# Kernel optimization log

Measured on AMD Instinct MI355X. Metric: run time of the kernel, lower is better.

The kernel has to match this reference:

```python
import jax, jax.numpy as jnp
import numpy as np

N = 100_000   # nodes
E = 640_000   # edges
H = 128       # hidden_dim
L = 4         # num_layers
C = 2         # num_classes
G = 128       # graphs in batch

def setup_inputs() -> dict:
    key = jax.random.key(0)
    ks = jax.random.split(key, 8)
    x = jax.random.randint(ks[0], (N, 1), 0, 2)
    edge_index = jax.random.randint(ks[1], (2, E), 0, N)
    batch = jnp.sort(jax.random.randint(ks[2], (N,), 0, G))
    embed = jax.random.normal(ks[3], (2, H), jnp.float32)
    Ws = jax.random.normal(ks[4], (L, H, H), jnp.float32) * (1.0 / np.sqrt(H))
    bs = jnp.zeros((L, H), jnp.float32)
    W_out = jax.random.normal(ks[5], (H, C), jnp.float32) * (1.0 / np.sqrt(H))
    b_out = jnp.zeros((C,), jnp.float32)
    return dict(x=x, edge_index=edge_index, batch=batch, embed=embed,
                Ws=Ws, bs=bs, W_out=W_out, b_out=b_out)

def reference(x, edge_index, batch, embed, Ws, bs, W_out, b_out):
    src, dst = edge_index[0], edge_index[1]
    # symmetric GCN normalization with self-loops (PyG GCNConv default)
    deg = jax.ops.segment_sum(jnp.ones(E, jnp.float32), dst, num_segments=N) + 1.0
    dinv = jax.lax.rsqrt(deg)
    enorm = (dinv[src] * dinv[dst])[:, None]   # per-edge norm
    snorm = (dinv * dinv)[:, None]             # self-loop norm

    h = embed[x[:, 0]]                          # [N, H] embedding lookup
    n_layers = Ws.shape[0]
    for l in range(n_layers):
        t = h @ Ws[l]                           # linear transform [N, H]
        agg = jax.ops.segment_sum(t[src] * enorm, dst, num_segments=N) \
              + t * snorm + bs[l]
        h = jax.nn.relu(agg) if l < n_layers - 1 else agg

    # global mean pool over graph ids
    counts = jax.ops.segment_sum(jnp.ones(N, jnp.float32), batch, num_segments=G)
    pooled = jax.ops.segment_sum(h, batch, num_segments=G) \
             / jnp.maximum(counts, 1.0)[:, None]   # [G, H]
    return pooled @ W_out + b_out                  # [G, C]
```

## Files before the change

kernel.cpp:

```cpp
#include <hip/hip_runtime.h>

typedef __attribute__((ext_vector_type(8))) short bf16x8;
typedef __attribute__((ext_vector_type(4))) float f32x4;
typedef __attribute__((ext_vector_type(2))) float f32x2;

__device__ inline unsigned short bf16_rtn(float f) {
  unsigned u = __float_as_uint(f);
  unsigned r = u + 0x7fffu + ((u >> 16) & 1u);
  return (unsigned short)(r >> 16);
}

__device__ inline void split_bf16(float f, unsigned short& hi, unsigned short& lo) {
  hi = bf16_rtn(f);
  float fh = __uint_as_float((unsigned)hi << 16);
  lo = bf16_rtn(f - fh);
}

__device__ inline float bf16_to_f(unsigned short v) {
  return __uint_as_float((unsigned)v << 16);
}

__device__ inline unsigned char f_to_fp8(float f) {
  int r = __builtin_amdgcn_cvt_pk_fp8_f32(f, f, 0, false);
  return (unsigned char)(r & 0xff);
}
__device__ inline f32x2 fp8x2_to_f(unsigned short v) {
  return __builtin_amdgcn_cvt_pk_f32_fp8((int)v, false);
}

__global__ void k_init(int* __restrict__ deg, int* __restrict__ gpz, int N, int M,
                       const float* __restrict__ Ws, const float* __restrict__ embed,
                       unsigned short* __restrict__ wphi,
                       unsigned short* __restrict__ wplo,
                       float* __restrict__ T,
                       unsigned char* __restrict__ t_a,
                       unsigned char* __restrict__ t_b) {
  int i = blockIdx.x * 256 + threadIdx.x;
  if (i < N) deg[i] = 0;
  if (i < M) gpz[i] = 0;
  int l = blockIdx.x;
  if (l < 3) {
    const float* W = Ws + (size_t)(l + 1) * 128 * 128;
    unsigned short* dh = wphi + (size_t)l * 16384;
    unsigned short* dl = wplo + (size_t)l * 16384;
    for (int idx = threadIdx.x; idx < 16384; idx += 256) {
      int j = idx & 7;
      int lane = (idx >> 3) & 63;
      int c = (idx >> 9) & 3;
      int ct = idx >> 11;
      int k = c * 32 + ((lane >> 4) * 8) + j;
      int n = ct * 16 + (lane & 15);
      unsigned short hi, lo;
      split_bf16(W[k * 128 + n], hi, lo);
      dh[idx] = hi;
      dl[idx] = lo;
    }
  } else if (l == 3) {
    int t = threadIdx.x;
    int r = t >> 7, c = t & 127;
    float acc = 0.f;
    for (int k = 0; k < 128; ++k)
      acc += embed[r * 128 + k] * Ws[k * 128 + c];
    T[r * 128 + c] = acc;
  } else if (l == 4) {
    int t = threadIdx.x;
    if (t < 32)      ((unsigned*)(t_a + (size_t)N * 128))[t] = 0u;
    else if (t < 64) ((unsigned*)(t_b + (size_t)N * 128))[t - 32] = 0u;
  }
}


__global__ void k_hist(const int* __restrict__ dst, int* __restrict__ deg,
                       int* __restrict__ posr, int E) {
  int e = blockIdx.x * 256 + threadIdx.x;
  if (e < E) posr[e] = atomicAdd(&deg[dst[e]], 1);
}

__global__ void k_scan1(const int* __restrict__ deg, int* __restrict__ rowptr,
                        int* __restrict__ bsum, float* __restrict__ dpk,
                        const int* __restrict__ x, const int* __restrict__ batch,
                        int* __restrict__ gstart, int* __restrict__ gend, int N) {
  __shared__ int s[256];
  int t = threadIdx.x;
  int i = blockIdx.x * 256 + t;
  int v = (i < N) ? deg[i] : 0;
  if (i < N) {
    float di = rsqrtf((float)v + 1.0f);
    dpk[i] = x[i] ? -di : di;
    int g = batch[i];
    if (i == 0 || batch[i - 1] != g) gstart[g] = i;
    if (i == N - 1 || batch[i + 1] != g) gend[g] = i + 1;
  }
  s[t] = v;
  __syncthreads();
  for (int off = 1; off < 256; off <<= 1) {
    int u = (t >= off) ? s[t - off] : 0;
    __syncthreads();
    s[t] += u;
    __syncthreads();
  }
  if (i < N) rowptr[i] = s[t] - v;
  if (t == 255) bsum[blockIdx.x] = s[255];
}

__global__ void k_scan2(const int* __restrict__ bsum, int* __restrict__ boff, int nb) {
  __shared__ int s[512];
  int t = threadIdx.x;
  int v = (t < nb) ? bsum[t] : 0;
  s[t] = v;
  __syncthreads();
  for (int off = 1; off < 512; off <<= 1) {
    int u = (t >= off) ? s[t - off] : 0;
    __syncthreads();
    s[t] += u;
    __syncthreads();
  }
  boff[t] = s[t] - v;
}

__global__ void k_scan3(int* __restrict__ rowptr, const int* __restrict__ boff,
                        int N, int E) {
  int i = blockIdx.x * 256 + threadIdx.x;
  if (i < N) rowptr[i] += boff[i >> 8];
  if (i == 0) rowptr[N] = E;
}

__global__ void k_scatter(const int* __restrict__ src, const int* __restrict__ dst,
                          const int* __restrict__ posr, const int* __restrict__ rowptr,
                          const float* __restrict__ dpk,
                          int2* __restrict__ epack, int E) {
  int e = blockIdx.x * 256 + threadIdx.x;
  if (e >= E) return;
  int s = src[e], d = dst[e];
  int pos = rowptr[d] + posr[e];
  epack[pos] = make_int2(s, __float_as_int(dpk[s]));
}


__device__ inline void acc16(float* a, uint4 p) {
  f32x2 v;
  v = __builtin_amdgcn_cvt_pk_f32_fp8((int)p.x, false); a[0]  += v.x; a[1]  += v.y;
  v = __builtin_amdgcn_cvt_pk_f32_fp8((int)p.x, true);  a[2]  += v.x; a[3]  += v.y;
  v = __builtin_amdgcn_cvt_pk_f32_fp8((int)p.y, false); a[4]  += v.x; a[5]  += v.y;
  v = __builtin_amdgcn_cvt_pk_f32_fp8((int)p.y, true);  a[6]  += v.x; a[7]  += v.y;
  v = __builtin_amdgcn_cvt_pk_f32_fp8((int)p.z, false); a[8]  += v.x; a[9]  += v.y;
  v = __builtin_amdgcn_cvt_pk_f32_fp8((int)p.z, true);  a[10] += v.x; a[11] += v.y;
  v = __builtin_amdgcn_cvt_pk_f32_fp8((int)p.w, false); a[12] += v.x; a[13] += v.y;
  v = __builtin_amdgcn_cvt_pk_f32_fp8((int)p.w, true);  a[14] += v.x; a[15] += v.y;
}

__device__ inline void gather8(const unsigned char* __restrict__ tin,
                               const int2* __restrict__ epack,
                               int r0, int deg, int l8, int N,
                               float* a) {
  int dcap = deg < 16 ? deg : 16;
  int slo = N, shi = N;
  if (2 * l8 < dcap)     slo = epack[r0 + 2 * l8].x;
  if (2 * l8 + 1 < dcap) shi = epack[r0 + 2 * l8 + 1].x;

  uint4 p[16];
  #pragma unroll
  for (int k = 0; k < 8; ++k) {
    int se = __shfl(slo, k, 8);
    int so = __shfl(shi, k, 8);
    p[2 * k]     = *(const uint4*)(tin + (size_t)((unsigned)se * 128u + ((unsigned)l8 << 4)));
    p[2 * k + 1] = *(const uint4*)(tin + (size_t)((unsigned)so * 128u + ((unsigned)l8 << 4)));
  }
  #pragma unroll
  for (int k = 0; k < 16; ++k) acc16(a, p[k]);

  if (__builtin_expect(deg > 16, 0)) {
    for (int e = r0 + 16; e < r0 + deg; ++e) {
      int s = epack[e].x;
      uint4 q = *(const uint4*)(tin + (size_t)((unsigned)s * 128u + ((unsigned)l8 << 4)));
      acc16(a, q);
    }
  }
}

__global__ __launch_bounds__(256)
void k_agg(const unsigned char* __restrict__ tin,
           const int* __restrict__ rowptr,
           const int2* __restrict__ epack,
           const float* __restrict__ dpk, const float* __restrict__ bvec,
           unsigned short* __restrict__ h, int N) {
  int lane = threadIdx.x & 63;
  int g8 = lane >> 3, l8 = lane & 7;
  int wid = (blockIdx.x * 256 + threadIdx.x) >> 6;
  int i = wid * 8 + g8;
  if (i >= N) return;
  int r0 = rowptr[i], r1 = rowptr[i + 1];
  uint4 ps = *(const uint4*)(tin + (size_t)i * 128 + (l8 << 4));
  float dp = dpk[i];

  float a[16];
  #pragma unroll
  for (int k = 0; k < 16; ++k) a[k] = 0.f;
  gather8(tin, epack, r0, r1 - r0, l8, N, a);
  acc16(a, ps);

  float di = fabsf(dp);
  const float4* bp = (const float4*)(bvec + 16 * l8);
  float4 b0 = bp[0], b1 = bp[1], b2 = bp[2], b3 = bp[3];
  float bb[16] = {b0.x, b0.y, b0.z, b0.w, b1.x, b1.y, b1.z, b1.w,
                  b2.x, b2.y, b2.z, b2.w, b3.x, b3.y, b3.z, b3.w};
  unsigned u[8];
  #pragma unroll
  for (int k = 0; k < 8; ++k) {
    float v0 = fmaxf(di * a[2 * k]     + bb[2 * k],     0.f);
    float v1 = fmaxf(di * a[2 * k + 1] + bb[2 * k + 1], 0.f);
    u[k] = (unsigned)bf16_rtn(v0) | ((unsigned)bf16_rtn(v1) << 16);
  }
  uint4* hp = (uint4*)(h + (size_t)i * 128 + 16 * l8);
  hp[0] = make_uint4(u[0], u[1], u[2], u[3]);
  hp[1] = make_uint4(u[4], u[5], u[6], u[7]);
}

__global__ __launch_bounds__(256)
void k_agg_pool(const unsigned char* __restrict__ tin,
                const int* __restrict__ rowptr,
                const int2* __restrict__ epack,
                const float* __restrict__ dpk, const float* __restrict__ bvec,
                const int* __restrict__ batch,
                float* __restrict__ pooled, int N) {
  __shared__ float sh[32][128];
  __shared__ int sg[32];
  int lane = threadIdx.x & 63;
  int g8 = lane >> 3, l8 = lane & 7;
  int nloc = (threadIdx.x >> 6) * 8 + g8;
  int i = blockIdx.x * 32 + nloc;
  if (threadIdx.x < 32) sg[threadIdx.x] = -1;
  __syncthreads();
  if (i < N) {
    int r0 = rowptr[i], r1 = rowptr[i + 1];
    uint4 ps = *(const uint4*)(tin + (size_t)i * 128 + (l8 << 4));
    float dp = dpk[i];

    float a[16];
    #pragma unroll
    for (int k = 0; k < 16; ++k) a[k] = 0.f;
    gather8(tin, epack, r0, r1 - r0, l8, N, a);
    acc16(a, ps);

    float di = fabsf(dp);
    const float4* bp = (const float4*)(bvec + 16 * l8);
    float4 b0 = bp[0], b1 = bp[1], b2 = bp[2], b3 = bp[3];
    float bb[16] = {b0.x, b0.y, b0.z, b0.w, b1.x, b1.y, b1.z, b1.w,
                    b2.x, b2.y, b2.z, b2.w, b3.x, b3.y, b3.z, b3.w};
    #pragma unroll
    for (int k = 0; k < 16; ++k)
      sh[nloc][16 * l8 + k] = di * a[k] + bb[k];
    if (l8 == 0) sg[nloc] = batch[i];
  }
  __syncthreads();
  if (threadIdx.x < 128) {
    int c = threadIdx.x;
    float acc = 0.f;
    int cur = sg[0];
    #pragma unroll
    for (int w2 = 0; w2 < 32; ++w2) {
      int gw = sg[w2];
      if (gw < 0) break;
      if (gw != cur) {
        atomicAdd(&pooled[cur * 128 + c], acc);
        acc = 0.f;
        cur = gw;
      }
      acc += sh[w2][c];
    }
    atomicAdd(&pooled[cur * 128 + c], acc);
  }
}

__global__ void k_gemm(const unsigned short* __restrict__ h,
                       const unsigned short* __restrict__ wphi,
                       const unsigned short* __restrict__ wplo,
                       const float* __restrict__ dpk,
                       unsigned char* __restrict__ tout, int N) {
  int wave = threadIdx.x >> 6;
  int lane = threadIdx.x & 63;
  int r0 = (blockIdx.x * 4 + wave) * 32;
  if (r0 >= N) return;
  int q = lane >> 4;
  int m = lane & 15;
  const bf16x8* bh_base = (const bf16x8*)wphi;
  const bf16x8* bl_base = (const bf16x8*)wplo;

  f32x4 acc[2][8];
  #pragma unroll
  for (int tt = 0; tt < 2; ++tt)
    #pragma unroll
    for (int ct = 0; ct < 8; ++ct)
      acc[tt][ct] = (f32x4){0.f, 0.f, 0.f, 0.f};

  for (int c = 0; c < 4; ++c) {
    bf16x8 a0 = *(const bf16x8*)(h + (size_t)(r0 + m) * 128 + c * 32 + q * 8);
    bf16x8 a1 = *(const bf16x8*)(h + (size_t)(r0 + 16 + m) * 128 + c * 32 + q * 8);
    #pragma unroll
    for (int ct = 0; ct < 8; ++ct) {
      bf16x8 bh = bh_base[(ct * 4 + c) * 64 + lane];
      bf16x8 bl = bl_base[(ct * 4 + c) * 64 + lane];
      acc[0][ct] = __builtin_amdgcn_mfma_f32_16x16x32_bf16(a0, bh, acc[0][ct], 0, 0, 0);
      acc[0][ct] = __builtin_amdgcn_mfma_f32_16x16x32_bf16(a0, bl, acc[0][ct], 0, 0, 0);
      acc[1][ct] = __builtin_amdgcn_mfma_f32_16x16x32_bf16(a1, bh, acc[1][ct], 0, 0, 0);
      acc[1][ct] = __builtin_amdgcn_mfma_f32_16x16x32_bf16(a1, bl, acc[1][ct], 0, 0, 0);
    }
  }

  #pragma unroll
  for (int tt = 0; tt < 2; ++tt)
    #pragma unroll
    for (int ct = 0; ct < 8; ++ct)
      #pragma unroll
      for (int r = 0; r < 4; ++r) {
        int row = r0 + tt * 16 + q * 4 + r;
        if (row < N) {
          float sc = fabsf(dpk[row]);
          tout[(size_t)row * 128 + ct * 16 + m] = f_to_fp8(sc * acc[tt][ct][r]);
        }
      }
}

__device__ inline void gemm_tile8(const unsigned short* hT,
                                  const unsigned short* __restrict__ wphi,
                                  const unsigned short* __restrict__ wplo,
                                  const float* __restrict__ dpk,
                                  unsigned char* __restrict__ tout, int i0, int N) {
  int ct = threadIdx.x >> 6;
  int lane = threadIdx.x & 63;
  int q = lane >> 4;
  int m = lane & 15;
  const bf16x8* bh_base = (const bf16x8*)wphi;
  const bf16x8* bl_base = (const bf16x8*)wplo;

  f32x4 acc0 = (f32x4){0.f, 0.f, 0.f, 0.f};
  f32x4 acc1 = (f32x4){0.f, 0.f, 0.f, 0.f};

  #pragma unroll
  for (int c = 0; c < 4; ++c) {
    bf16x8 a0 = *(const bf16x8*)(hT + (m) * 136 + c * 32 + q * 8);
    bf16x8 a1 = *(const bf16x8*)(hT + (16 + m) * 136 + c * 32 + q * 8);
    bf16x8 bh = bh_base[(ct * 4 + c) * 64 + lane];
    bf16x8 bl = bl_base[(ct * 4 + c) * 64 + lane];
    acc0 = __builtin_amdgcn_mfma_f32_16x16x32_bf16(a0, bh, acc0, 0, 0, 0);
    acc0 = __builtin_amdgcn_mfma_f32_16x16x32_bf16(a0, bl, acc0, 0, 0, 0);
    acc1 = __builtin_amdgcn_mfma_f32_16x16x32_bf16(a1, bh, acc1, 0, 0, 0);
    acc1 = __builtin_amdgcn_mfma_f32_16x16x32_bf16(a1, bl, acc1, 0, 0, 0);
  }

  #pragma unroll
  for (int r = 0; r < 4; ++r) {
    int row0 = i0 + q * 4 + r;
    int row1 = row0 + 16;
    if (row0 < N) {
      float sc = fabsf(dpk[row0]);
      tout[(size_t)row0 * 128 + ct * 16 + m] = f_to_fp8(sc * acc0[r]);
    }
    if (row1 < N) {
      float sc = fabsf(dpk[row1]);
      tout[(size_t)row1 * 128 + ct * 16 + m] = f_to_fp8(sc * acc1[r]);
    }
  }
}

__global__ __launch_bounds__(512)
void k_l1_gemm(const int* __restrict__ rowptr,
               const int2* __restrict__ epack,
               const float* __restrict__ dpk, const float* __restrict__ T,
               const float* __restrict__ b0,
               const unsigned short* __restrict__ wphi,
               const unsigned short* __restrict__ wplo,
               unsigned char* __restrict__ tout, int N) {
  __shared__ unsigned short hT[32 * 136];
  int wave = threadIdx.x >> 6;
  int lane = threadIdx.x & 63;
  int i0 = blockIdx.x * 32;

  for (int j = wave * 4; j < wave * 4 + 4; ++j) {
    int i = i0 + j;
    if (i >= N) break;
    int r0 = rowptr[i], r1 = rowptr[i + 1];
    float sabs = 0.f, sneg = 0.f;
    for (int e = r0 + lane; e < r1; e += 64) {
      float wv = __int_as_float(epack[e].y);
      float aw = fabsf(wv);
      sabs += aw;
      if (wv < 0.f) sneg += aw;
    }
    for (int mm = 32; mm >= 1; mm >>= 1) {
      sabs += __shfl_xor(sabs, mm, 64);
      sneg += __shfl_xor(sneg, mm, 64);
    }
    float dp = dpk[i];
    float di = fabsf(dp);
    float sn = di * di;
    float c1 = di * sneg;
    float c0 = di * (sabs - sneg);
    if (dp < 0.f) c1 += sn; else c0 += sn;
    float v0 = fmaxf(c0 * T[2 * lane]     + c1 * T[128 + 2 * lane]     + b0[2 * lane],     0.f);
    float v1 = fmaxf(c0 * T[2 * lane + 1] + c1 * T[128 + 2 * lane + 1] + b0[2 * lane + 1], 0.f);
    *(unsigned*)&hT[j * 136 + 2 * lane] = (unsigned)bf16_rtn(v0) | ((unsigned)bf16_rtn(v1) << 16);
  }
  __syncthreads();
  gemm_tile8(hT, wphi, wplo, dpk, tout, i0, N);
}

__global__ void k_out(const float* __restrict__ pooled, const int* __restrict__ gstart,
                      const int* __restrict__ gend, const float* __restrict__ W_out,
                      const float* __restrict__ b_out, float* __restrict__ out, int G) {
  __shared__ float sp[128];
  int g = blockIdx.x;
  int j = threadIdx.x;
  float cnt = (float)(gend[g] - gstart[g]);
  sp[j] = pooled[g * 128 + j] / fmaxf(cnt, 1.f);
  __syncthreads();
  if (j < 2) {
    float o = b_out[j];
    for (int k = 0; k < 128; ++k)
      o += sp[k] * W_out[k * 2 + j];
    out[g * 2 + j] = o;
  }
}

extern "C" void kernel_launch(void* const* d_in, const int* in_sizes, int n_in,
                              void* d_out, int out_size, void* d_ws, size_t ws_size,
                              hipStream_t stream) {
  const int*   x     = (const int*)d_in[0];
  const int*   ei    = (const int*)d_in[1];
  const int*   batch = (const int*)d_in[2];
  const float* embed = (const float*)d_in[3];
  const float* Ws    = (const float*)d_in[4];
  const float* bs    = (const float*)d_in[5];
  const float* W_out = (const float*)d_in[6];
  const float* b_out = (const float*)d_in[7];
  float* out = (float*)d_out;

  int N = in_sizes[2];
  int E = in_sizes[1] / 2;
  int G = out_size / 2;

  const int* src = ei;
  const int* dst = ei + E;

  char* w = (char*)d_ws;
  auto alloc = [&](size_t bytes) {
    char* p = w;
    w += (bytes + 255) & ~(size_t)255;
    return p;
  };
  int*   deg    = (int*)  alloc((size_t)N * 4);
  float* dpk    = (float*)alloc((size_t)N * 4);
  int*   rowptr = (int*)  alloc((size_t)(N + 1) * 4);
  int*   posr   = (int*)  alloc((size_t)E * 4);
  int*   bsum   = (int*)  alloc(512 * 4);
  int*   boff   = (int*)  alloc(512 * 4);
  int*   gstart = (int*)  alloc((size_t)G * 4);
  int*   gend   = (int*)  alloc((size_t)G * 4);
  float* pooled = (float*)alloc((size_t)G * 128 * 4);
  float* T      = (float*)alloc(256 * 4);
  unsigned short* wphi = (unsigned short*)alloc((size_t)3 * 16384 * 2);
  unsigned short* wplo = (unsigned short*)alloc((size_t)3 * 16384 * 2);
  int2*  epack  = (int2*) alloc((size_t)E * 8);
  unsigned short* h = (unsigned short*)alloc((size_t)N * 128 * 2);
  unsigned char* t_a = (unsigned char*)alloc((size_t)(N + 1) * 128);
  unsigned char* t_b = (unsigned char*)alloc((size_t)(N + 1) * 128);

  int nbN = (N + 255) / 256;
  int nbE = (E + 255) / 256;
  int ntile = (N + 31) / 32;
  int nagg = (N + 31) / 32;
  int ngemm = (N + 127) / 128;
  int M = G * 130;

  k_init<<<nbN, 256, 0, stream>>>(deg, gstart, N, M, Ws, embed, wphi, wplo, T, t_a, t_b);
  k_hist<<<nbE, 256, 0, stream>>>(dst, deg, posr, E);
  k_scan1<<<nbN, 256, 0, stream>>>(deg, rowptr, bsum, dpk, x, batch, gstart, gend, N);
  k_scan2<<<1, 512, 0, stream>>>(bsum, boff, nbN);
  k_scan3<<<nbN, 256, 0, stream>>>(rowptr, boff, N, E);
  k_scatter<<<nbE, 256, 0, stream>>>(src, dst, posr, rowptr, dpk, epack, E);

  k_l1_gemm<<<ntile, 512, 0, stream>>>(rowptr, epack, dpk, T, bs,
                                       wphi, wplo, t_a, N);
  k_agg<<<nagg, 256, 0, stream>>>(t_a, rowptr, epack, dpk, bs + 128, h, N);
  k_gemm<<<ngemm, 256, 0, stream>>>(h, wphi + 16384, wplo + 16384, dpk, t_b, N);
  k_agg<<<nagg, 256, 0, stream>>>(t_b, rowptr, epack, dpk, bs + 256, h, N);
  k_gemm<<<ngemm, 256, 0, stream>>>(h, wphi + 32768, wplo + 32768, dpk, t_a, N);
  k_agg_pool<<<nagg, 256, 0, stream>>>(t_a, rowptr, epack, dpk, bs + 384,
                                       batch, pooled, N);
  k_out<<<G, 128, 0, stream>>>(pooled, gstart, gend, W_out, b_out, out, G);
}
```

Measured before the change: 288.1 us.

## Fuse aggregation and next-layer GEMM via shared-memory tile of h

Merges the per-layer aggregation kernel with the following linear-transform GEMM. Each block aggregates 32 nodes, writes the bf16 activations to a padded LDS tile, then four waves each compute two 16-column output tiles with MFMA and write fp8 results. This removes the global round trip of the bf16 h buffer and two kernel launches per forward pass. In exchange, every block re-reads the weight fragments and there is a block-wide barrier between gather and GEMM.

```diff
diff --git a/kernel.cpp b/kernel.cpp
--- a/kernel.cpp
+++ b/kernel.cpp
@@ -179,41 +179,97 @@
 }
 
 __global__ __launch_bounds__(256)
-void k_agg(const unsigned char* __restrict__ tin,
-           const int* __restrict__ rowptr,
-           const int2* __restrict__ epack,
-           const float* __restrict__ dpk, const float* __restrict__ bvec,
-           unsigned short* __restrict__ h, int N) {
+void k_agg_gemm(const unsigned char* __restrict__ tin,
+                const int* __restrict__ rowptr,
+                const int2* __restrict__ epack,
+                const float* __restrict__ dpk, const float* __restrict__ bvec,
+                const unsigned short* __restrict__ wphi,
+                const unsigned short* __restrict__ wplo,
+                unsigned char* __restrict__ tout, int N) {
+  __shared__ unsigned short hT[32 * 136];
   int lane = threadIdx.x & 63;
+  int wave = threadIdx.x >> 6;
   int g8 = lane >> 3, l8 = lane & 7;
-  int wid = (blockIdx.x * 256 + threadIdx.x) >> 6;
-  int i = wid * 8 + g8;
-  if (i >= N) return;
-  int r0 = rowptr[i], r1 = rowptr[i + 1];
-  uint4 ps = *(const uint4*)(tin + (size_t)i * 128 + (l8 << 4));
-  float dp = dpk[i];
-
-  float a[16];
-  #pragma unroll
-  for (int k = 0; k < 16; ++k) a[k] = 0.f;
-  gather8(tin, epack, r0, r1 - r0, l8, N, a);
-  acc16(a, ps);
-
-  float di = fabsf(dp);
-  const float4* bp = (const float4*)(bvec + 16 * l8);
-  float4 b0 = bp[0], b1 = bp[1], b2 = bp[2], b3 = bp[3];
-  float bb[16] = {b0.x, b0.y, b0.z, b0.w, b1.x, b1.y, b1.z, b1.w,
-                  b2.x, b2.y, b2.z, b2.w, b3.x, b3.y, b3.z, b3.w};
+  int nloc = wave * 8 + g8;
+  int i0 = blockIdx.x * 32;
+  int i = i0 + nloc;
+
   unsigned u[8];
-  #pragma unroll
-  for (int k = 0; k < 8; ++k) {
-    float v0 = fmaxf(di * a[2 * k]     + bb[2 * k],     0.f);
-    float v1 = fmaxf(di * a[2 * k + 1] + bb[2 * k + 1], 0.f);
-    u[k] = (unsigned)bf16_rtn(v0) | ((unsigned)bf16_rtn(v1) << 16);
-  }
-  uint4* hp = (uint4*)(h + (size_t)i * 128 + 16 * l8);
-  hp[0] = make_uint4(u[0], u[1], u[2], u[3]);
-  hp[1] = make_uint4(u[4], u[5], u[6], u[7]);
+  if (i < N) {
+    int r0 = rowptr[i], r1 = rowptr[i + 1];
+    uint4 ps = *(const uint4*)(tin + (size_t)i * 128 + (l8 << 4));
+    float dp = dpk[i];
+
+    float a[16];
+    #pragma unroll
+    for (int k = 0; k < 16; ++k) a[k] = 0.f;
+    gather8(tin, epack, r0, r1 - r0, l8, N, a);
+    acc16(a, ps);
+
+    float di = fabsf(dp);
+    const float4* bp = (const float4*)(bvec + 16 * l8);
+    float4 b0 = bp[0], b1 = bp[1], b2 = bp[2], b3 = bp[3];
+    float bb[16] = {b0.x, b0.y, b0.z, b0.w, b1.x, b1.y, b1.z, b1.w,
+                    b2.x, b2.y, b2.z, b2.w, b3.x, b3.y, b3.z, b3.w};
+    #pragma unroll
+    for (int k = 0; k < 8; ++k) {
+      float v0 = fmaxf(di * a[2 * k]     + bb[2 * k],     0.f);
+      float v1 = fmaxf(di * a[2 * k + 1] + bb[2 * k + 1], 0.f);
+      u[k] = (unsigned)bf16_rtn(v0) | ((unsigned)bf16_rtn(v1) << 16);
+    }
+  } else {
+    #pragma unroll
+    for (int k = 0; k < 8; ++k) u[k] = 0u;
+  }
+  {
+    uint4* hp = (uint4*)&hT[nloc * 136 + 16 * l8];
+    hp[0] = make_uint4(u[0], u[1], u[2], u[3]);
+    hp[1] = make_uint4(u[4], u[5], u[6], u[7]);
+  }
+  __syncthreads();
+
+  int q = lane >> 4;
+  int m = lane & 15;
+  const bf16x8* bh_base = (const bf16x8*)wphi;
+  const bf16x8* bl_base = (const bf16x8*)wplo;
+
+  f32x4 acc[2][2];
+  #pragma unroll
+  for (int tt = 0; tt < 2; ++tt)
+    #pragma unroll
+    for (int ctl = 0; ctl < 2; ++ctl)
+      acc[tt][ctl] = (f32x4){0.f, 0.f, 0.f, 0.f};
+
+  #pragma unroll
+  for (int c = 0; c < 4; ++c) {
+    bf16x8 a0 = *(const bf16x8*)(hT + m * 136 + c * 32 + q * 8);
+    bf16x8 a1 = *(const bf16x8*)(hT + (16 + m) * 136 + c * 32 + q * 8);
+    #pragma unroll
+    for (int ctl = 0; ctl < 2; ++ctl) {
+      int ct = wave * 2 + ctl;
+      bf16x8 bh = bh_base[(ct * 4 + c) * 64 + lane];
+      bf16x8 bl = bl_base[(ct * 4 + c) * 64 + lane];
+      acc[0][ctl] = __builtin_amdgcn_mfma_f32_16x16x32_bf16(a0, bh, acc[0][ctl], 0, 0, 0);
+      acc[0][ctl] = __builtin_amdgcn_mfma_f32_16x16x32_bf16(a0, bl, acc[0][ctl], 0, 0, 0);
+      acc[1][ctl] = __builtin_amdgcn_mfma_f32_16x16x32_bf16(a1, bh, acc[1][ctl], 0, 0, 0);
+      acc[1][ctl] = __builtin_amdgcn_mfma_f32_16x16x32_bf16(a1, bl, acc[1][ctl], 0, 0, 0);
+    }
+  }
+
+  #pragma unroll
+  for (int tt = 0; tt < 2; ++tt)
+    #pragma unroll
+    for (int ctl = 0; ctl < 2; ++ctl) {
+      int ct = wave * 2 + ctl;
+      #pragma unroll
+      for (int r = 0; r < 4; ++r) {
+        int row = i0 + tt * 16 + q * 4 + r;
+        if (row < N) {
+          float sc = fabsf(dpk[row]);
+          tout[(size_t)row * 128 + ct * 16 + m] = f_to_fp8(sc * acc[tt][ctl][r]);
+        }
+      }
+    }
 }
 
 __global__ __launch_bounds__(256)
@@ -270,55 +326,6 @@
     }
     atomicAdd(&pooled[cur * 128 + c], acc);
   }
-}
-
-__global__ void k_gemm(const unsigned short* __restrict__ h,
-                       const unsigned short* __restrict__ wphi,
-                       const unsigned short* __restrict__ wplo,
-                       const float* __restrict__ dpk,
-                       unsigned char* __restrict__ tout, int N) {
-  int wave = threadIdx.x >> 6;
-  int lane = threadIdx.x & 63;
-  int r0 = (blockIdx.x * 4 + wave) * 32;
-  if (r0 >= N) return;
-  int q = lane >> 4;
-  int m = lane & 15;
-  const bf16x8* bh_base = (const bf16x8*)wphi;
-  const bf16x8* bl_base = (const bf16x8*)wplo;
-
-  f32x4 acc[2][8];
-  #pragma unroll
-  for (int tt = 0; tt < 2; ++tt)
-    #pragma unroll
-    for (int ct = 0; ct < 8; ++ct)
-      acc[tt][ct] = (f32x4){0.f, 0.f, 0.f, 0.f};
-
-  for (int c = 0; c < 4; ++c) {
-    bf16x8 a0 = *(const bf16x8*)(h + (size_t)(r0 + m) * 128 + c * 32 + q * 8);
-    bf16x8 a1 = *(const bf16x8*)(h + (size_t)(r0 + 16 + m) * 128 + c * 32 + q * 8);
-    #pragma unroll
-    for (int ct = 0; ct < 8; ++ct) {
-      bf16x8 bh = bh_base[(ct * 4 + c) * 64 + lane];
-      bf16x8 bl = bl_base[(ct * 4 + c) * 64 + lane];
-      acc[0][ct] = __builtin_amdgcn_mfma_f32_16x16x32_bf16(a0, bh, acc[0][ct], 0, 0, 0);
-      acc[0][ct] = __builtin_amdgcn_mfma_f32_16x16x32_bf16(a0, bl, acc[0][ct], 0, 0, 0);
-      acc[1][ct] = __builtin_amdgcn_mfma_f32_16x16x32_bf16(a1, bh, acc[1][ct], 0, 0, 0);
-      acc[1][ct] = __builtin_amdgcn_mfma_f32_16x16x32_bf16(a1, bl, acc[1][ct], 0, 0, 0);
-    }
-  }
-
-  #pragma unroll
-  for (int tt = 0; tt < 2; ++tt)
-    #pragma unroll
-    for (int ct = 0; ct < 8; ++ct)
-      #pragma unroll
-      for (int r = 0; r < 4; ++r) {
-        int row = r0 + tt * 16 + q * 4 + r;
-        if (row < N) {
-          float sc = fabsf(dpk[row]);
-          tout[(size_t)row * 128 + ct * 16 + m] = f_to_fp8(sc * acc[tt][ct][r]);
-        }
-      }
 }
 
 __device__ inline void gemm_tile8(const unsigned short* hT,
@@ -461,7 +468,6 @@
   unsigned short* wphi = (unsigned short*)alloc((size_t)3 * 16384 * 2);
   unsigned short* wplo = (unsigned short*)alloc((size_t)3 * 16384 * 2);
   int2*  epack  = (int2*) alloc((size_t)E * 8);
-  unsigned short* h = (unsigned short*)alloc((size_t)N * 128 * 2);
   unsigned char* t_a = (unsigned char*)alloc((size_t)(N + 1) * 128);
   unsigned char* t_b = (unsigned char*)alloc((size_t)(N + 1) * 128);
 
@@ -469,7 +475,6 @@
   int nbE = (E + 255) / 256;
   int ntile = (N + 31) / 32;
   int nagg = (N + 31) / 32;
-  int ngemm = (N + 127) / 128;
   int M = G * 130;
 
   k_init<<<nbN, 256, 0, stream>>>(deg, gstart, N, M, Ws, embed, wphi, wplo, T, t_a, t_b);
@@ -481,10 +486,10 @@
 
   k_l1_gemm<<<ntile, 512, 0, stream>>>(rowptr, epack, dpk, T, bs,
                                        wphi, wplo, t_a, N);
-  k_agg<<<nagg, 256, 0, stream>>>(t_a, rowptr, epack, dpk, bs + 128, h, N);
-  k_gemm<<<ngemm, 256, 0, stream>>>(h, wphi + 16384, wplo + 16384, dpk, t_b, N);
-  k_agg<<<nagg, 256, 0, stream>>>(t_b, rowptr, epack, dpk, bs + 256, h, N);
-  k_gemm<<<ngemm, 256, 0, stream>>>(h, wphi + 32768, wplo + 32768, dpk, t_a, N);
+  k_agg_gemm<<<nagg, 256, 0, stream>>>(t_a, rowptr, epack, dpk, bs + 128,
+                                       wphi + 16384, wplo + 16384, t_b, N);
+  k_agg_gemm<<<nagg, 256, 0, stream>>>(t_b, rowptr, epack, dpk, bs + 256,
+                                       wphi + 32768, wplo + 32768, t_a, N);
   k_agg_pool<<<nagg, 256, 0, stream>>>(t_a, rowptr, epack, dpk, bs + 384,
                                        batch, pooled, N);
   k_out<<<G, 128, 0, stream>>>(pooled, gstart, gend, W_out, b_out, out, G);
```

Result: no change. 292.8 us (+1.6%).

## Add separate source-index array and shrink aggregation blocks to one wave

Applied to the files above, without the earlier changes.

The scatter kernel now also writes a compact int array of source indices in CSR order. The aggregation kernels read that array instead of the 8-byte packed edge records, halving the index bytes they fetch. The agg and agg_pool kernels are also relaunched with 64-thread single-wave blocks covering 8 nodes each, which lets waves schedule independently. The cost is an extra E-sized write in scatter, and the pool kernel does more atomics because each block now holds 8 nodes instead of 32.

```diff
diff --git a/kernel.cpp b/kernel.cpp
--- a/kernel.cpp
+++ b/kernel.cpp
@@ -128,12 +128,13 @@
 __global__ void k_scatter(const int* __restrict__ src, const int* __restrict__ dst,
                           const int* __restrict__ posr, const int* __restrict__ rowptr,
                           const float* __restrict__ dpk,
-                          int2* __restrict__ epack, int E) {
+                          int2* __restrict__ epack, int* __restrict__ esrc, int E) {
   int e = blockIdx.x * 256 + threadIdx.x;
   if (e >= E) return;
   int s = src[e], d = dst[e];
   int pos = rowptr[d] + posr[e];
   epack[pos] = make_int2(s, __float_as_int(dpk[s]));
+  esrc[pos] = s;
 }
 
 
@@ -150,13 +151,13 @@
 }
 
 __device__ inline void gather8(const unsigned char* __restrict__ tin,
-                               const int2* __restrict__ epack,
+                               const int* __restrict__ esrc,
                                int r0, int deg, int l8, int N,
                                float* a) {
   int dcap = deg < 16 ? deg : 16;
   int slo = N, shi = N;
-  if (2 * l8 < dcap)     slo = epack[r0 + 2 * l8].x;
-  if (2 * l8 + 1 < dcap) shi = epack[r0 + 2 * l8 + 1].x;
+  if (2 * l8 < dcap)     slo = esrc[r0 + 2 * l8];
+  if (2 * l8 + 1 < dcap) shi = esrc[r0 + 2 * l8 + 1];
 
   uint4 p[16];
   #pragma unroll
@@ -171,23 +172,22 @@
 
   if (__builtin_expect(deg > 16, 0)) {
     for (int e = r0 + 16; e < r0 + deg; ++e) {
-      int s = epack[e].x;
+      int s = esrc[e];
       uint4 q = *(const uint4*)(tin + (size_t)((unsigned)s * 128u + ((unsigned)l8 << 4)));
       acc16(a, q);
     }
   }
 }
 
-__global__ __launch_bounds__(256)
+__global__ __launch_bounds__(64)
 void k_agg(const unsigned char* __restrict__ tin,
            const int* __restrict__ rowptr,
-           const int2* __restrict__ epack,
+           const int* __restrict__ esrc,
            const float* __restrict__ dpk, const float* __restrict__ bvec,
            unsigned short* __restrict__ h, int N) {
-  int lane = threadIdx.x & 63;
+  int lane = threadIdx.x;
   int g8 = lane >> 3, l8 = lane & 7;
-  int wid = (blockIdx.x * 256 + threadIdx.x) >> 6;
-  int i = wid * 8 + g8;
+  int i = blockIdx.x * 8 + g8;
   if (i >= N) return;
   int r0 = rowptr[i], r1 = rowptr[i + 1];
   uint4 ps = *(const uint4*)(tin + (size_t)i * 128 + (l8 << 4));
@@ -196,7 +196,7 @@
   float a[16];
   #pragma unroll
   for (int k = 0; k < 16; ++k) a[k] = 0.f;
-  gather8(tin, epack, r0, r1 - r0, l8, N, a);
+  gather8(tin, esrc, r0, r1 - r0, l8, N, a);
   acc16(a, ps);
 
   float di = fabsf(dp);
@@ -216,20 +216,19 @@
   hp[1] = make_uint4(u[4], u[5], u[6], u[7]);
 }
 
-__global__ __launch_bounds__(256)
+__global__ __launch_bounds__(64)
 void k_agg_pool(const unsigned char* __restrict__ tin,
                 const int* __restrict__ rowptr,
-                const int2* __restrict__ epack,
+                const int* __restrict__ esrc,
                 const float* __restrict__ dpk, const float* __restrict__ bvec,
                 const int* __restrict__ batch,
                 float* __restrict__ pooled, int N) {
-  __shared__ float sh[32][128];
-  __shared__ int sg[32];
-  int lane = threadIdx.x & 63;
+  __shared__ float sh[8][128];
+  __shared__ int sg[8];
+  int lane = threadIdx.x;
   int g8 = lane >> 3, l8 = lane & 7;
-  int nloc = (threadIdx.x >> 6) * 8 + g8;
-  int i = blockIdx.x * 32 + nloc;
-  if (threadIdx.x < 32) sg[threadIdx.x] = -1;
+  int i = blockIdx.x * 8 + g8;
+  if (lane < 8) sg[lane] = -1;
   __syncthreads();
   if (i < N) {
     int r0 = rowptr[i], r1 = rowptr[i + 1];
@@ -239,7 +238,7 @@
     float a[16];
     #pragma unroll
     for (int k = 0; k < 16; ++k) a[k] = 0.f;
-    gather8(tin, epack, r0, r1 - r0, l8, N, a);
+    gather8(tin, esrc, r0, r1 - r0, l8, N, a);
     acc16(a, ps);
 
     float di = fabsf(dp);
@@ -249,16 +248,17 @@
                     b2.x, b2.y, b2.z, b2.w, b3.x, b3.y, b3.z, b3.w};
     #pragma unroll
     for (int k = 0; k < 16; ++k)
-      sh[nloc][16 * l8 + k] = di * a[k] + bb[k];
-    if (l8 == 0) sg[nloc] = batch[i];
-  }
-  __syncthreads();
-  if (threadIdx.x < 128) {
-    int c = threadIdx.x;
+      sh[g8][16 * l8 + k] = di * a[k] + bb[k];
+    if (l8 == 0) sg[g8] = batch[i];
+  }
+  __syncthreads();
+  #pragma unroll
+  for (int cc = 0; cc < 2; ++cc) {
+    int c = threadIdx.x + 64 * cc;
     float acc = 0.f;
     int cur = sg[0];
     #pragma unroll
-    for (int w2 = 0; w2 < 32; ++w2) {
+    for (int w2 = 0; w2 < 8; ++w2) {
       int gw = sg[w2];
       if (gw < 0) break;
       if (gw != cur) {
@@ -268,7 +268,7 @@
       }
       acc += sh[w2][c];
     }
-    atomicAdd(&pooled[cur * 128 + c], acc);
+    if (cur >= 0) atomicAdd(&pooled[cur * 128 + c], acc);
   }
 }
 
@@ -461,6 +461,7 @@
   unsigned short* wphi = (unsigned short*)alloc((size_t)3 * 16384 * 2);
   unsigned short* wplo = (unsigned short*)alloc((size_t)3 * 16384 * 2);
   int2*  epack  = (int2*) alloc((size_t)E * 8);
+  int*   esrc   = (int*)  alloc((size_t)E * 4);
   unsigned short* h = (unsigned short*)alloc((size_t)N * 128 * 2);
   unsigned char* t_a = (unsigned char*)alloc((size_t)(N + 1) * 128);
   unsigned char* t_b = (unsigned char*)alloc((size_t)(N + 1) * 128);
@@ -468,7 +469,7 @@
   int nbN = (N + 255) / 256;
   int nbE = (E + 255) / 256;
   int ntile = (N + 31) / 32;
-  int nagg = (N + 31) / 32;
+  int nagg = (N + 7) / 8;
   int ngemm = (N + 127) / 128;
   int M = G * 130;
 
@@ -477,15 +478,15 @@
   k_scan1<<<nbN, 256, 0, stream>>>(deg, rowptr, bsum, dpk, x, batch, gstart, gend, N);
   k_scan2<<<1, 512, 0, stream>>>(bsum, boff, nbN);
   k_scan3<<<nbN, 256, 0, stream>>>(rowptr, boff, N, E);
-  k_scatter<<<nbE, 256, 0, stream>>>(src, dst, posr, rowptr, dpk, epack, E);
+  k_scatter<<<nbE, 256, 0, stream>>>(src, dst, posr, rowptr, dpk, epack, esrc, E);
 
   k_l1_gemm<<<ntile, 512, 0, stream>>>(rowptr, epack, dpk, T, bs,
                                        wphi, wplo, t_a, N);
-  k_agg<<<nagg, 256, 0, stream>>>(t_a, rowptr, epack, dpk, bs + 128, h, N);
+  k_agg<<<nagg, 64, 0, stream>>>(t_a, rowptr, esrc, dpk, bs + 128, h, N);
   k_gemm<<<ngemm, 256, 0, stream>>>(h, wphi + 16384, wplo + 16384, dpk, t_b, N);
-  k_agg<<<nagg, 256, 0, stream>>>(t_b, rowptr, epack, dpk, bs + 256, h, N);
+  k_agg<<<nagg, 64, 0, stream>>>(t_b, rowptr, esrc, dpk, bs + 256, h, N);
   k_gemm<<<ngemm, 256, 0, stream>>>(h, wphi + 32768, wplo + 32768, dpk, t_a, N);
-  k_agg_pool<<<nagg, 256, 0, stream>>>(t_a, rowptr, epack, dpk, bs + 384,
-                                       batch, pooled, N);
+  k_agg_pool<<<nagg, 64, 0, stream>>>(t_a, rowptr, esrc, dpk, bs + 384,
+                                      batch, pooled, N);
   k_out<<<G, 128, 0, stream>>>(pooled, gstart, gend, W_out, b_out, out, G);
 }
```

New measurement: 294.5 us. +2.2%, slower.

## Fuse CSR preprocessing kernels into one cooperative kernel with grid syncs

Applied to the files above, without the earlier changes.

Merges the six preprocessing kernels (init, histogram, three-pass scan, scatter) into a single cooperative launch of 1024 blocks that separates phases with grid-wide syncs. The aim is to remove the launch overhead and inter-kernel gaps of several small kernels. The cost is five grid barriers and grid-stride loops, and the single-block scan phase leaves the other blocks idle while they wait. The cooperative launch also requires all 1024 blocks to be co-resident on the device.

```diff
diff --git a/kernel.cpp b/kernel.cpp
--- a/kernel.cpp
+++ b/kernel.cpp
@@ -1,4 +1,7 @@
 #include <hip/hip_runtime.h>
+#include <hip/hip_cooperative_groups.h>
+
+namespace cg = cooperative_groups;
 
 typedef __attribute__((ext_vector_type(8))) short bf16x8;
 typedef __attribute__((ext_vector_type(4))) float f32x4;
@@ -16,124 +19,121 @@
   lo = bf16_rtn(f - fh);
 }
 
-__device__ inline float bf16_to_f(unsigned short v) {
-  return __uint_as_float((unsigned)v << 16);
-}
-
 __device__ inline unsigned char f_to_fp8(float f) {
   int r = __builtin_amdgcn_cvt_pk_fp8_f32(f, f, 0, false);
   return (unsigned char)(r & 0xff);
 }
-__device__ inline f32x2 fp8x2_to_f(unsigned short v) {
-  return __builtin_amdgcn_cvt_pk_f32_fp8((int)v, false);
-}
-
-__global__ void k_init(int* __restrict__ deg, int* __restrict__ gpz, int N, int M,
-                       const float* __restrict__ Ws, const float* __restrict__ embed,
-                       unsigned short* __restrict__ wphi,
-                       unsigned short* __restrict__ wplo,
-                       float* __restrict__ T,
-                       unsigned char* __restrict__ t_a,
-                       unsigned char* __restrict__ t_b) {
-  int i = blockIdx.x * 256 + threadIdx.x;
-  if (i < N) deg[i] = 0;
-  if (i < M) gpz[i] = 0;
-  int l = blockIdx.x;
-  if (l < 3) {
-    const float* W = Ws + (size_t)(l + 1) * 128 * 128;
-    unsigned short* dh = wphi + (size_t)l * 16384;
-    unsigned short* dl = wplo + (size_t)l * 16384;
-    for (int idx = threadIdx.x; idx < 16384; idx += 256) {
-      int j = idx & 7;
-      int lane = (idx >> 3) & 63;
-      int c = (idx >> 9) & 3;
-      int ct = idx >> 11;
-      int k = c * 32 + ((lane >> 4) * 8) + j;
-      int n = ct * 16 + (lane & 15);
-      unsigned short hi, lo;
-      split_bf16(W[k * 128 + n], hi, lo);
-      dh[idx] = hi;
-      dl[idx] = lo;
-    }
-  } else if (l == 3) {
-    int t = threadIdx.x;
-    int r = t >> 7, c = t & 127;
+
+__global__ __launch_bounds__(256, 4)
+void k_csr(const int* __restrict__ x, const int* __restrict__ ei,
+           const int* __restrict__ batch,
+           const float* __restrict__ Ws, const float* __restrict__ embed,
+           int* __restrict__ deg, int* __restrict__ gpz,
+           int N, int M, int E,
+           unsigned short* __restrict__ wphi, unsigned short* __restrict__ wplo,
+           float* __restrict__ T,
+           unsigned char* __restrict__ t_a, unsigned char* __restrict__ t_b,
+           float* __restrict__ dpk, int* __restrict__ rowptr,
+           int* __restrict__ bsum, int* __restrict__ boff,
+           int* __restrict__ gstart, int* __restrict__ gend,
+           int* __restrict__ posr, int2* __restrict__ epack) {
+  cg::grid_group grid = cg::this_grid();
+  __shared__ int sdata[256];
+  __shared__ int s2[512];
+
+  const int tid = blockIdx.x * 256 + threadIdx.x;
+  const int nth = gridDim.x * 256;
+  const int* src = ei;
+  const int* dst = ei + E;
+  const int nbN = (N + 255) >> 8;
+
+  for (int i = tid; i < N; i += nth) deg[i] = 0;
+  for (int i = tid; i < M; i += nth) gpz[i] = 0;
+  for (int idx = tid; idx < 3 * 16384; idx += nth) {
+    int l = idx >> 14;
+    int rr = idx & 16383;
+    const float* W = Ws + (size_t)(l + 1) * 16384;
+    int j = rr & 7;
+    int lane = (rr >> 3) & 63;
+    int c = (rr >> 9) & 3;
+    int ct = rr >> 11;
+    int k = c * 32 + ((lane >> 4) * 8) + j;
+    int n = ct * 16 + (lane & 15);
+    unsigned short hi, lo;
+    split_bf16(W[k * 128 + n], hi, lo);
+    wphi[(size_t)l * 16384 + rr] = hi;
+    wplo[(size_t)l * 16384 + rr] = lo;
+  }
+  for (int idx = tid; idx < 256; idx += nth) {
+    int r = idx >> 7, c = idx & 127;
     float acc = 0.f;
     for (int k = 0; k < 128; ++k)
       acc += embed[r * 128 + k] * Ws[k * 128 + c];
     T[r * 128 + c] = acc;
-  } else if (l == 4) {
+  }
+  for (int idx = tid; idx < 64; idx += nth) {
+    if (idx < 32) ((unsigned*)(t_a + (size_t)N * 128))[idx] = 0u;
+    else          ((unsigned*)(t_b + (size_t)N * 128))[idx - 32] = 0u;
+  }
+  grid.sync();
+
+  for (int e = tid; e < E; e += nth) posr[e] = atomicAdd(&deg[dst[e]], 1);
+  grid.sync();
+
+  for (int s = blockIdx.x; s < nbN; s += gridDim.x) {
     int t = threadIdx.x;
-    if (t < 32)      ((unsigned*)(t_a + (size_t)N * 128))[t] = 0u;
-    else if (t < 64) ((unsigned*)(t_b + (size_t)N * 128))[t - 32] = 0u;
-  }
-}
-
-
-__global__ void k_hist(const int* __restrict__ dst, int* __restrict__ deg,
-                       int* __restrict__ posr, int E) {
-  int e = blockIdx.x * 256 + threadIdx.x;
-  if (e < E) posr[e] = atomicAdd(&deg[dst[e]], 1);
-}
-
-__global__ void k_scan1(const int* __restrict__ deg, int* __restrict__ rowptr,
-                        int* __restrict__ bsum, float* __restrict__ dpk,
-                        const int* __restrict__ x, const int* __restrict__ batch,
-                        int* __restrict__ gstart, int* __restrict__ gend, int N) {
-  __shared__ int s[256];
-  int t = threadIdx.x;
-  int i = blockIdx.x * 256 + t;
-  int v = (i < N) ? deg[i] : 0;
-  if (i < N) {
-    float di = rsqrtf((float)v + 1.0f);
-    dpk[i] = x[i] ? -di : di;
-    int g = batch[i];
-    if (i == 0 || batch[i - 1] != g) gstart[g] = i;
-    if (i == N - 1 || batch[i + 1] != g) gend[g] = i + 1;
-  }
-  s[t] = v;
-  __syncthreads();
-  for (int off = 1; off < 256; off <<= 1) {
-    int u = (t >= off) ? s[t - off] : 0;
+    int i = s * 256 + t;
+    int v = (i < N) ? deg[i] : 0;
+    if (i < N) {
+      float di = rsqrtf((float)v + 1.0f);
+      dpk[i] = x[i] ? -di : di;
+      int g = batch[i];
+      if (i == 0 || batch[i - 1] != g) gstart[g] = i;
+      if (i == N - 1 || batch[i + 1] != g) gend[g] = i + 1;
+    }
+    sdata[t] = v;
     __syncthreads();
-    s[t] += u;
+    for (int off = 1; off < 256; off <<= 1) {
+      int u = (t >= off) ? sdata[t - off] : 0;
+      __syncthreads();
+      sdata[t] += u;
+      __syncthreads();
+    }
+    if (i < N) rowptr[i] = sdata[t] - v;
+    if (t == 255) bsum[s] = sdata[255];
     __syncthreads();
   }
-  if (i < N) rowptr[i] = s[t] - v;
-  if (t == 255) bsum[blockIdx.x] = s[255];
-}
-
-__global__ void k_scan2(const int* __restrict__ bsum, int* __restrict__ boff, int nb) {
-  __shared__ int s[512];
-  int t = threadIdx.x;
-  int v = (t < nb) ? bsum[t] : 0;
-  s[t] = v;
-  __syncthreads();
-  for (int off = 1; off < 512; off <<= 1) {
-    int u = (t >= off) ? s[t - off] : 0;
+  grid.sync();
+
+  if (blockIdx.x == 0) {
+    int t = threadIdx.x;
+    int v0 = (t < nbN) ? bsum[t] : 0;
+    int v1 = (t + 256 < nbN) ? bsum[t + 256] : 0;
+    s2[t] = v0;
+    s2[t + 256] = v1;
     __syncthreads();
-    s[t] += u;
-    __syncthreads();
-  }
-  boff[t] = s[t] - v;
-}
-
-__global__ void k_scan3(int* __restrict__ rowptr, const int* __restrict__ boff,
-                        int N, int E) {
-  int i = blockIdx.x * 256 + threadIdx.x;
-  if (i < N) rowptr[i] += boff[i >> 8];
-  if (i == 0) rowptr[N] = E;
-}
-
-__global__ void k_scatter(const int* __restrict__ src, const int* __restrict__ dst,
-                          const int* __restrict__ posr, const int* __restrict__ rowptr,
-                          const float* __restrict__ dpk,
-                          int2* __restrict__ epack, int E) {
-  int e = blockIdx.x * 256 + threadIdx.x;
-  if (e >= E) return;
-  int s = src[e], d = dst[e];
-  int pos = rowptr[d] + posr[e];
-  epack[pos] = make_int2(s, __float_as_int(dpk[s]));
+    for (int off = 1; off < 512; off <<= 1) {
+      int u0 = (t >= off) ? s2[t - off] : 0;
+      int u1 = (t + 256 >= off) ? s2[t + 256 - off] : 0;
+      __syncthreads();
+      s2[t] += u0;
+      s2[t + 256] += u1;
+      __syncthreads();
+    }
+    boff[t] = s2[t] - v0;
+    boff[t + 256] = s2[t + 256] - v1;
+  }
+  grid.sync();
+
+  for (int i = tid; i < N; i += nth) rowptr[i] += boff[i >> 8];
+  if (tid == 0) rowptr[N] = E;
+  grid.sync();
+
+  for (int e = tid; e < E; e += nth) {
+    int s = src[e], d = dst[e];
+    int pos = rowptr[d] + posr[e];
+    epack[pos] = make_int2(s, __float_as_int(dpk[s]));
+  }
 }
 
 
@@ -438,9 +438,6 @@
   int N = in_sizes[2];
   int E = in_sizes[1] / 2;
   int G = out_size / 2;
-
-  const int* src = ei;
-  const int* dst = ei + E;
 
   char* w = (char*)d_ws;
   auto alloc = [&](size_t bytes) {
@@ -465,19 +462,19 @@
   unsigned char* t_a = (unsigned char*)alloc((size_t)(N + 1) * 128);
   unsigned char* t_b = (unsigned char*)alloc((size_t)(N + 1) * 128);
 
-  int nbN = (N + 255) / 256;
-  int nbE = (E + 255) / 256;
   int ntile = (N + 31) / 32;
   int nagg = (N + 31) / 32;
   int ngemm = (N + 127) / 128;
   int M = G * 130;
 
-  k_init<<<nbN, 256, 0, stream>>>(deg, gstart, N, M, Ws, embed, wphi, wplo, T, t_a, t_b);
-  k_hist<<<nbE, 256, 0, stream>>>(dst, deg, posr, E);
-  k_scan1<<<nbN, 256, 0, stream>>>(deg, rowptr, bsum, dpk, x, batch, gstart, gend, N);
-  k_scan2<<<1, 512, 0, stream>>>(bsum, boff, nbN);
-  k_scan3<<<nbN, 256, 0, stream>>>(rowptr, boff, N, E);
-  k_scatter<<<nbE, 256, 0, stream>>>(src, dst, posr, rowptr, dpk, epack, E);
+  void* cargs[] = {
+    (void*)&x, (void*)&ei, (void*)&batch, (void*)&Ws, (void*)&embed,
+    (void*)&deg, (void*)&gstart, (void*)&N, (void*)&M, (void*)&E,
+    (void*)&wphi, (void*)&wplo, (void*)&T, (void*)&t_a, (void*)&t_b,
+    (void*)&dpk, (void*)&rowptr, (void*)&bsum, (void*)&boff,
+    (void*)&gstart, (void*)&gend, (void*)&posr, (void*)&epack
+  };
+  hipLaunchCooperativeKernel((void*)k_csr, dim3(1024), dim3(256), cargs, 0, stream);
 
   k_l1_gemm<<<ntile, 512, 0, stream>>>(rowptr, epack, dpk, T, bs,
                                        wphi, wplo, t_a, N);
```

New measurement: 778.5 us. +170.2%, slower.
